# Kernel tuning notes

Hardware: AMD Instinct MI355X
Metric: run time of the kernel (lower is better)

Reference implementation:

```python
import jax, jax.numpy as jnp
import numpy as np

N_NODES = 100000
N_EDGES = 1600000
D = 128
N_LAYERS = 3


def _sage_layer(x, src, dst, Wl, Wr, bias, n_nodes):
    # mean aggregation of source-node features at destination nodes
    msg_sum = jax.ops.segment_sum(x[src], dst, num_segments=n_nodes)  # [N, D]
    cnt = jax.ops.segment_sum(jnp.ones((src.shape[0], 1), x.dtype), dst,
                              num_segments=n_nodes)  # [N, 1]
    mean = msg_sum / jnp.maximum(cnt, 1.0)
    # PyG SAGEConv: out = lin_l(aggr) + lin_r(x); lin_l carries the bias
    return mean @ Wl + x @ Wr + bias


def setup_inputs() -> dict:
    key = jax.random.key(0)
    k1, k2, k3, k4, k5 = jax.random.split(key, 5)
    scale = 1.0 / np.sqrt(D)
    x = jax.random.normal(k1, (N_NODES, D), dtype=jnp.float32)
    edge_index = jax.random.randint(k2, (2, N_EDGES), 0, N_NODES, dtype=jnp.int64)
    W_agg = jax.random.normal(k3, (N_LAYERS, D, D), dtype=jnp.float32) * scale
    W_root = jax.random.normal(k4, (N_LAYERS, D, D), dtype=jnp.float32) * scale
    b = jax.random.normal(k5, (N_LAYERS, D), dtype=jnp.float32) * scale
    return {"x": x, "edge_index": edge_index, "W_agg": W_agg,
            "W_root": W_root, "b": b}


def reference(x, edge_index, W_agg, W_root, b):
    src, dst = edge_index[0], edge_index[1]
    n = x.shape[0]
    # hidden layers: conv -> (dropout=identity in eval) -> relu
    for i in range(N_LAYERS - 1):
        x = _sage_layer(x, src, dst, W_agg[i], W_root[i], b[i], n)
        x = jax.nn.relu(x)
    # final layer: no relu
    x = _sage_layer(x, src, dst, W_agg[-1], W_root[-1], b[-1], n)
    return x
```

## Files before the change

### kernel.cpp

```cpp
#include <hip/hip_runtime.h>
#include <stdint.h>

#define D 128
#define CHUNK 6400

typedef __attribute__((ext_vector_type(8))) __bf16 bf16x8;
typedef __attribute__((ext_vector_type(4))) __bf16 bf16x4;
typedef __attribute__((ext_vector_type(4))) float f32x4;

__global__ void detect_idx(const void* ei, int* flag, int n_nodes) {
    if (blockIdx.x == 0 && threadIdx.x == 0) {
        const long long* p = (const long long*)ei;
        int is64 = 1;
        for (int i = 0; i < 64; ++i) {
            long long v = p[i];
            if (v < 0 || v >= (long long)n_nodes) { is64 = 0; break; }
        }
        *flag = is64;
    }
}

__global__ __launch_bounds__(256) void convert_pack(
        const void* __restrict__ ei, const int* __restrict__ flag,
        unsigned int* __restrict__ eword, unsigned char* __restrict__ gb,
        int* __restrict__ bcnt, int nE) {
    __shared__ int l[256];
    l[threadIdx.x] = 0;
    __syncthreads();
    bool is64 = *flag != 0;
    int stride = gridDim.x * 256;
    for (int e = blockIdx.x * 256 + threadIdx.x; e < nE; e += stride) {
        int s, d;
        if (is64) {
            const long long* p = (const long long*)ei;
            s = (int)p[e];
            d = (int)p[(size_t)nE + e];
        } else {
            const int* p = (const int*)ei;
            s = p[e];
            d = p[nE + e];
        }
        eword[e] = ((unsigned)s << 9) | (unsigned)(d & 511);
        gb[e] = (unsigned char)(d >> 9);
        atomicAdd(&l[d >> 9], 1);
    }
    __syncthreads();
    int v = l[threadIdx.x];
    if (v) atomicAdd(&bcnt[threadIdx.x], v);
}

__global__ void bucket_scan(const int* __restrict__ bcnt, int* __restrict__ bstart,
                            int* __restrict__ bcur, int G, int nE,
                            int* __restrict__ offsets, int n) {
    __shared__ int s[256];
    int t = threadIdx.x;
    int v = (t < G) ? bcnt[t] : 0;
    s[t] = v;
    __syncthreads();
    for (int off = 1; off < 256; off <<= 1) {
        int u = 0;
        if (t >= off) u = s[t - off];
        __syncthreads();
        if (t >= off) s[t] += u;
        __syncthreads();
    }
    if (t < G) { int ex = s[t] - v; bstart[t] = ex; bcur[t] = ex; }
    if (t == 0) offsets[n] = nE;
}

__global__ __launch_bounds__(256) void bucket_fill2(
        const unsigned int* __restrict__ eword, const unsigned char* __restrict__ gb,
        int* __restrict__ bcur, unsigned int* __restrict__ ebuf, int nE) {
    __shared__ unsigned int lw[CHUNK];
    __shared__ unsigned char lg[CHUNK];
    __shared__ int lcnt[256], lbase[256], lcur[256];
    int e0 = blockIdx.x * CHUNK;
    int cnt = nE - e0;
    if (cnt > CHUNK) cnt = CHUNK;
    if (cnt < 0) cnt = 0;
    for (int i = threadIdx.x; i < cnt; i += 256) {
        lw[i] = eword[e0 + i];
        lg[i] = gb[e0 + i];
    }
    lcnt[threadIdx.x] = 0;
    __syncthreads();
    for (int i = threadIdx.x; i < cnt; i += 256)
        atomicAdd(&lcnt[lg[i]], 1);
    __syncthreads();
    int c = lcnt[threadIdx.x];
    if (c > 0) lbase[threadIdx.x] = atomicAdd(&bcur[threadIdx.x], c);
    lcur[threadIdx.x] = 0;
    __syncthreads();
    for (int i = threadIdx.x; i < cnt; i += 256) {
        int g = lg[i];
        int p = lbase[g] + atomicAdd(&lcur[g], 1);
        ebuf[p] = lw[i];
    }
}

__global__ __launch_bounds__(256) void bucket_scatter2(
        const unsigned int* __restrict__ ebuf,
        const int* __restrict__ bstart, const int* __restrict__ bcnt,
        int* __restrict__ offsets, int* __restrict__ csr, int n) {
    __shared__ int ncnt[512], nofs[512], ps[256];
    int g = blockIdx.x;
    int base = bstart[g];
    int cnt = bcnt[g];
    int n0 = g << 9;
    int nr = n - n0; if (nr > 512) nr = 512;
    for (int i = threadIdx.x; i < 512; i += 256) ncnt[i] = 0;
    __syncthreads();
    for (int i = threadIdx.x; i < cnt; i += 256)
        atomicAdd(&ncnt[ebuf[base + i] & 511], 1);
    __syncthreads();
    int t = threadIdx.x;
    int c0 = ncnt[2 * t], c1 = ncnt[2 * t + 1];
    ps[t] = c0 + c1;
    __syncthreads();
    for (int off = 1; off < 256; off <<= 1) {
        int u = 0;
        if (t >= off) u = ps[t - off];
        __syncthreads();
        if (t >= off) ps[t] += u;
        __syncthreads();
    }
    int pex = ps[t] - (c0 + c1);
    nofs[2 * t] = pex;
    nofs[2 * t + 1] = pex + c0;
    __syncthreads();
    for (int i = threadIdx.x; i < nr; i += 256)
        offsets[n0 + i] = base + nofs[i];
    for (int i = threadIdx.x; i < 512; i += 256) ncnt[i] = 0;
    __syncthreads();
    for (int i = threadIdx.x; i < cnt; i += 256) {
        unsigned int w = ebuf[base + i];
        int d = w & 511;
        int p = base + nofs[d] + atomicAdd(&ncnt[d], 1);
        csr[p] = (int)(w >> 9);
    }
}

__global__ void build_wt(const float* __restrict__ Wa, const float* __restrict__ Wr,
                         __bf16* __restrict__ WtHi, __bf16* __restrict__ WtLo) {
    int idx = blockIdx.x * 256 + threadIdx.x;
    if (idx >= 3 * 128 * 256) return;
    int L = idx / (128 * 256);
    int rem = idx % (128 * 256);
    int c = rem / 256;
    int k = rem % 256;
    float v = (k < 128) ? Wa[((size_t)L * 128 + k) * 128 + c]
                        : Wr[((size_t)L * 128 + (k - 128)) * 128 + c];
    __bf16 h = (__bf16)v;
    __bf16 l = (__bf16)(v - (float)h);
    WtHi[idx] = h;
    WtLo[idx] = l;
}

__global__ void cvt_x(const float* __restrict__ x, __bf16* __restrict__ a,
                      int total8) {
    int i = blockIdx.x * 256 + threadIdx.x;
    if (i >= total8) return;
    const float4* p = (const float4*)(x + (size_t)i * 8);
    float4 v0 = p[0], v1 = p[1];
    float vv[8] = {v0.x, v0.y, v0.z, v0.w, v1.x, v1.y, v1.z, v1.w};
    bf16x8 h;
    #pragma unroll
    for (int j = 0; j < 8; ++j) h[j] = (__bf16)vv[j];
    *(bf16x8*)(a + (size_t)i * 8) = h;
}

__global__ __launch_bounds__(256) void quant_act(
        const __bf16* __restrict__ act, unsigned char* __restrict__ q,
        float* __restrict__ scl, int n) {
    int row = (blockIdx.x * blockDim.x + threadIdx.x) >> 4;
    int l8 = (threadIdx.x & 15) << 3;
    if (row >= n) return;
    bf16x8 v = *(const bf16x8*)(act + (size_t)row * D + l8);
    float f[8];
    float m = 0.f;
    #pragma unroll
    for (int j = 0; j < 8; ++j) {
        f[j] = (float)v[j];
        m = fmaxf(m, fabsf(f[j]));
    }
    #pragma unroll
    for (int off = 8; off >= 1; off >>= 1)
        m = fmaxf(m, __shfl_xor(m, off));
    float scale = m * (1.0f / 127.0f);
    float inv = (m > 0.f) ? 127.0f / m : 0.f;
    unsigned int a = 0, b = 0;
    #pragma unroll
    for (int j = 0; j < 4; ++j) {
        unsigned int u = (unsigned int)(__float2int_rn(f[j] * inv) + 128);
        a |= u << (8 * j);
    }
    #pragma unroll
    for (int j = 0; j < 4; ++j) {
        unsigned int u = (unsigned int)(__float2int_rn(f[4 + j] * inv) + 128);
        b |= u << (8 * j);
    }
    *(int2*)(q + (size_t)row * D + l8) = make_int2((int)a, (int)b);
    if ((threadIdx.x & 15) == 0) scl[row] = scale;
}

__global__ __launch_bounds__(256) void agg_mean6(
        const unsigned char* __restrict__ q, const float* __restrict__ scl,
        const int* __restrict__ csr, const int* __restrict__ offs,
        __bf16* __restrict__ mean, int n) {
    int node = (blockIdx.x * blockDim.x + threadIdx.x) >> 4;
    int l8 = (threadIdx.x & 15) << 3;
    if (node >= n) return;
    int beg = offs[node], end = offs[node + 1];
    float acc[8] = {0.f, 0.f, 0.f, 0.f, 0.f, 0.f, 0.f, 0.f};
    float S = 0.f;
    int i = beg;
    for (; i + 8 <= end; i += 8) {
        int2 v[8]; float s[8];
        #pragma unroll
        for (int u = 0; u < 8; ++u) {
            int src = csr[i + u];
            v[u] = *(const int2*)(q + (size_t)src * D + l8);
            s[u] = scl[src];
        }
        #pragma unroll
        for (int u = 0; u < 8; ++u) {
            unsigned int a = (unsigned int)v[u].x, b = (unsigned int)v[u].y;
            float sv = s[u];
            S += sv;
            acc[0] += (float)(a & 255u) * sv;
            acc[1] += (float)((a >> 8) & 255u) * sv;
            acc[2] += (float)((a >> 16) & 255u) * sv;
            acc[3] += (float)(a >> 24) * sv;
            acc[4] += (float)(b & 255u) * sv;
            acc[5] += (float)((b >> 8) & 255u) * sv;
            acc[6] += (float)((b >> 16) & 255u) * sv;
            acc[7] += (float)(b >> 24) * sv;
        }
    }
    for (; i + 4 <= end; i += 4) {
        int2 v[4]; float s[4];
        #pragma unroll
        for (int u = 0; u < 4; ++u) {
            int src = csr[i + u];
            v[u] = *(const int2*)(q + (size_t)src * D + l8);
            s[u] = scl[src];
        }
        #pragma unroll
        for (int u = 0; u < 4; ++u) {
            unsigned int a = (unsigned int)v[u].x, b = (unsigned int)v[u].y;
            float sv = s[u];
            S += sv;
            acc[0] += (float)(a & 255u) * sv;
            acc[1] += (float)((a >> 8) & 255u) * sv;
            acc[2] += (float)((a >> 16) & 255u) * sv;
            acc[3] += (float)(a >> 24) * sv;
            acc[4] += (float)(b & 255u) * sv;
            acc[5] += (float)((b >> 8) & 255u) * sv;
            acc[6] += (float)((b >> 16) & 255u) * sv;
            acc[7] += (float)(b >> 24) * sv;
        }
    }
    for (; i < end; ++i) {
        int src = csr[i];
        int2 v = *(const int2*)(q + (size_t)src * D + l8);
        float sv = scl[src];
        unsigned int a = (unsigned int)v.x, b = (unsigned int)v.y;
        S += sv;
        acc[0] += (float)(a & 255u) * sv;
        acc[1] += (float)((a >> 8) & 255u) * sv;
        acc[2] += (float)((a >> 16) & 255u) * sv;
        acc[3] += (float)(a >> 24) * sv;
        acc[4] += (float)(b & 255u) * sv;
        acc[5] += (float)((b >> 8) & 255u) * sv;
        acc[6] += (float)((b >> 16) & 255u) * sv;
        acc[7] += (float)(b >> 24) * sv;
    }
    int deg = end - beg;
    float inv = 1.0f / (float)(deg > 1 ? deg : 1);
    bf16x8 h;
    #pragma unroll
    for (int j = 0; j < 8; ++j)
        h[j] = (__bf16)((acc[j] - 128.0f * S) * inv);
    *(bf16x8*)(mean + (size_t)node * D + l8) = h;
}

__global__ __launch_bounds__(512, 4) void sage_gemm8(
        const __bf16* __restrict__ mean, const __bf16* __restrict__ act,
        const __bf16* __restrict__ WtHi, const __bf16* __restrict__ WtLo,
        const float* __restrict__ bias,
        __bf16* __restrict__ oB, float* __restrict__ oF,
        int n, int mode, int npairs) {
    __shared__ __align__(16) char sA[2][2][8192];
    __shared__ __align__(16) char sC[2][8192];
    int tid  = threadIdx.x;
    int wave = tid >> 6;
    int lane = tid & 63;
    int r16  = lane & 15;
    int kg   = lane >> 4;
    int colbase = wave * 16;

    bf16x8 BH[8], BL[8];
    #pragma unroll
    for (int c8 = 0; c8 < 8; ++c8) {
        size_t o = (size_t)(colbase + r16) * 256 + c8 * 32 + kg * 8;
        BH[c8] = *(const bf16x8*)(WtHi + o);
        BL[c8] = *(const bf16x8*)(WtLo + o);
    }
    float4 bv = *(const float4*)(bias + colbase + kg * 4);

    int xm = (r16 & 7) << 4;
    int kb[8];
    #pragma unroll
    for (int c8 = 0; c8 < 8; ++c8)
        kb[c8] = r16 * 512 + ((c8 * 64 + kg * 16) ^ xm);

    int srow = tid >> 5;
    int sc16 = tid & 31;
    int sdst = srow * 512 + ((sc16 * 16) ^ ((srow & 7) << 4));

    auto stage_load = [&](int p, int half, int4& r) {
        int grow = p * 32 + half * 16 + srow;
        if (grow < n) {
            const __bf16* src = (sc16 < 16)
                ? (mean + (size_t)grow * D + sc16 * 8)
                : (act  + (size_t)grow * D + (sc16 - 16) * 8);
            r = *(const int4*)src;
        } else {
            r = make_int4(0, 0, 0, 0);
        }
    };

    int pstride = gridDim.x;
    int p = blockIdx.x;

    {
        int4 r0 = make_int4(0,0,0,0), r1 = make_int4(0,0,0,0);
        if (p < npairs) { stage_load(p, 0, r0); stage_load(p, 1, r1); }
        *(int4*)(sA[0][0] + sdst) = r0;
        *(int4*)(sA[0][1] + sdst) = r1;
    }
    __syncthreads();
    int cur = 0;

    for (; p < npairs; p += pstride) {
        int pn = p + pstride;
        bool hasnext = pn < npairs;
        int4 n0, n1;
        if (hasnext) { stage_load(pn, 0, n0); stage_load(pn, 1, n1); }

        f32x4 aH0 = (f32x4){0.f,0.f,0.f,0.f}, aL0 = aH0;
        f32x4 aH1 = aH0, aL1 = aH0;
        const char* b0 = sA[cur][0];
        const char* b1 = sA[cur][1];
        #pragma unroll
        for (int c8 = 0; c8 < 8; ++c8) {
            bf16x8 a0 = *(const bf16x8*)(b0 + kb[c8]);
            bf16x8 a1 = *(const bf16x8*)(b1 + kb[c8]);
            aH0 = __builtin_amdgcn_mfma_f32_16x16x32_bf16(BH[c8], a0, aH0, 0, 0, 0);
            aH1 = __builtin_amdgcn_mfma_f32_16x16x32_bf16(BH[c8], a1, aH1, 0, 0, 0);
            aL0 = __builtin_amdgcn_mfma_f32_16x16x32_bf16(BL[c8], a0, aL0, 0, 0, 0);
            aL1 = __builtin_amdgcn_mfma_f32_16x16x32_bf16(BL[c8], a1, aL1, 0, 0, 0);
        }

        __syncthreads();
        if (hasnext) {
            *(int4*)(sA[cur ^ 1][0] + sdst) = n0;
            *(int4*)(sA[cur ^ 1][1] + sdst) = n1;
        }

        #pragma unroll
        for (int h = 0; h < 2; ++h) {
            f32x4 a = h ? (aH1 + aL1) : (aH0 + aL0);
            float v0 = a[0] + bv.x;
            float v1 = a[1] + bv.y;
            float v2 = a[2] + bv.z;
            float v3 = a[3] + bv.w;
            if (mode == 0) {
                v0 = fmaxf(v0, 0.f); v1 = fmaxf(v1, 0.f);
                v2 = fmaxf(v2, 0.f); v3 = fmaxf(v3, 0.f);
                bf16x4 h4;
                h4[0] = (__bf16)v0; h4[1] = (__bf16)v1;
                h4[2] = (__bf16)v2; h4[3] = (__bf16)v3;
                *(bf16x4*)(sC[h] + r16 * 256 + (colbase + kg * 4) * 2) = h4;
            } else {
                *(f32x4*)(sC[h] + r16 * 512 + (colbase + kg * 4) * 4) =
                    (f32x4){v0, v1, v2, v3};
            }
        }
        __syncthreads();

        if (mode == 0) {
            int rr = tid >> 4, c16 = tid & 15;
            int grow = p * 32 + rr;
            if (grow < n) {
                int4 h = *(const int4*)(sC[rr >> 4] + (rr & 15) * 256 + c16 * 16);
                *(int4*)(oB + (size_t)grow * D + c16 * 8) = h;
            }
        } else {
            #pragma unroll
            for (int pass = 0; pass < 2; ++pass) {
                int chunk = pass * 512 + tid;
                int rr = chunk >> 5, c = chunk & 31;
                int grow = p * 32 + rr;
                if (grow < n) {
                    f32x4 f = *(const f32x4*)(sC[rr >> 4] + (rr & 15) * 512 + c * 16);
                    *(f32x4*)(oF + (size_t)grow * D + c * 4) = f;
                }
            }
        }
        cur ^= 1;
    }
}

extern "C" void kernel_launch(void* const* d_in, const int* in_sizes, int n_in,
                              void* d_out, int out_size, void* d_ws, size_t ws_size,
                              hipStream_t stream) {
    const float* x  = (const float*)d_in[0];
    const void*  ei = d_in[1];
    const float* Wa = (const float*)d_in[2];
    const float* Wr = (const float*)d_in[3];
    const float* bb = (const float*)d_in[4];
    float* outp = (float*)d_out;

    int n  = in_sizes[0] / D;
    int nE = in_sizes[1] / 2;
    int G  = (n + 511) >> 9;

    char* ws = (char*)d_ws;
    size_t off = 0;
    auto alloc = [&](size_t bytes) -> char* {
        char* p = ws + off;
        off = (off + bytes + 255) & ~(size_t)255;
        return p;
    };
    int* flag            = (int*)alloc(4);
    unsigned int* eword  = (unsigned int*)alloc((size_t)nE * 4);
    unsigned char* gbuf  = (unsigned char*)alloc((size_t)nE);
    unsigned int* ebuf   = (unsigned int*)alloc((size_t)nE * 4);
    int* offsets         = (int*)alloc(((size_t)n + 1) * 4);
    int* csr_src         = (int*)alloc((size_t)nE * 4);
    int* bcnt            = (int*)alloc(1024);
    int* bstart          = (int*)alloc(1024);
    int* bcur            = (int*)alloc(1024);
    __bf16* actA         = (__bf16*)alloc((size_t)n * D * 2);
    __bf16* actB         = (__bf16*)alloc((size_t)n * D * 2);
    __bf16* meanP        = (__bf16*)alloc((size_t)n * D * 2);
    unsigned char* qpl   = (unsigned char*)alloc((size_t)n * D);
    float* scl           = (float*)alloc((size_t)n * 4);
    __bf16* WtHi         = (__bf16*)alloc((size_t)3 * 128 * 256 * 2);
    __bf16* WtLo         = (__bf16*)alloc((size_t)3 * 128 * 256 * 2);
    (void)ws_size; (void)n_in; (void)out_size;

    const int B = 256;

    hipLaunchKernelGGL(detect_idx, dim3(1), dim3(64), 0, stream, ei, flag, n);
    hipMemsetAsync(bcnt, 0, 1024, stream);
    hipLaunchKernelGGL(convert_pack, dim3(512), dim3(B), 0, stream,
                       ei, flag, eword, gbuf, bcnt, nE);
    hipLaunchKernelGGL(build_wt, dim3(384), dim3(256), 0, stream, Wa, Wr, WtHi, WtLo);
    int total8 = n * D / 8;
    hipLaunchKernelGGL(cvt_x, dim3((total8 + 255) / 256), dim3(256), 0, stream,
                       x, actA, total8);

    hipLaunchKernelGGL(bucket_scan, dim3(1), dim3(B), 0, stream,
                       bcnt, bstart, bcur, G, nE, offsets, n);
    hipLaunchKernelGGL(bucket_fill2, dim3((nE + CHUNK - 1) / CHUNK), dim3(B), 0, stream,
                       eword, gbuf, bcur, ebuf, nE);
    hipLaunchKernelGGL(bucket_scatter2, dim3(G), dim3(B), 0, stream,
                       ebuf, bstart, bcnt, offsets, csr_src, n);

    int row_blocks = (n * 16 + B - 1) / B;
    int npairs = (n + 31) / 32;
    int gemm_grid = 512;
    const int WSTRIDE = 128 * 256;

    hipLaunchKernelGGL(quant_act, dim3(row_blocks), dim3(B), 0, stream,
                       actA, qpl, scl, n);
    hipLaunchKernelGGL(agg_mean6, dim3(row_blocks), dim3(B), 0, stream,
                       qpl, scl, csr_src, offsets, meanP, n);
    hipLaunchKernelGGL(sage_gemm8, dim3(gemm_grid), dim3(512), 0, stream,
                       meanP, actA, WtHi + 0 * WSTRIDE, WtLo + 0 * WSTRIDE,
                       bb + 0 * D, actB, outp, n, 0, npairs);

    hipLaunchKernelGGL(quant_act, dim3(row_blocks), dim3(B), 0, stream,
                       actB, qpl, scl, n);
    hipLaunchKernelGGL(agg_mean6, dim3(row_blocks), dim3(B), 0, stream,
                       qpl, scl, csr_src, offsets, meanP, n);
    hipLaunchKernelGGL(sage_gemm8, dim3(gemm_grid), dim3(512), 0, stream,
                       meanP, actB, WtHi + 1 * WSTRIDE, WtLo + 1 * WSTRIDE,
                       bb + 1 * D, actA, outp, n, 0, npairs);

    hipLaunchKernelGGL(quant_act, dim3(row_blocks), dim3(B), 0, stream,
                       actA, qpl, scl, n);
    hipLaunchKernelGGL(agg_mean6, dim3(row_blocks), dim3(B), 0, stream,
                       qpl, scl, csr_src, offsets, meanP, n);
    hipLaunchKernelGGL(sage_gemm8, dim3(gemm_grid), dim3(512), 0, stream,
                       meanP, actA, WtHi + 2 * WSTRIDE, WtLo + 2 * WSTRIDE,
                       bb + 2 * D, actB, outp, n, 1, npairs);
}
```

Before: 311.1 us.

## Fuse int8 activation quantization into input conversion and GEMM epilogue

Removes the three standalone quant_act launches. The first quantization now happens inside the fp32-to-bf16 input conversion, and the later ones inside the GEMM's mode-0 epilogue, which quantizes the bf16 tile it has just written. This avoids re-reading each layer's activations from global memory and the extra launch overhead. It also XOR-swizzles the epilogue's shared-memory staging buffer to cut LDS bank conflicts, at the cost of extra ALU work in the GEMM epilogue.

```diff
diff --git a/kernel.cpp b/kernel.cpp
--- a/kernel.cpp
+++ b/kernel.cpp
@@ -156,51 +156,39 @@
     WtLo[idx] = l;
 }
 
-__global__ void cvt_x(const float* __restrict__ x, __bf16* __restrict__ a,
-                      int total8) {
+__global__ __launch_bounds__(256) void cvt_x_q(
+        const float* __restrict__ x, __bf16* __restrict__ a,
+        unsigned char* __restrict__ q, float* __restrict__ scl, int total8) {
     int i = blockIdx.x * 256 + threadIdx.x;
     if (i >= total8) return;
+    int row = i >> 4;
+    int c16 = i & 15;
     const float4* p = (const float4*)(x + (size_t)i * 8);
     float4 v0 = p[0], v1 = p[1];
     float vv[8] = {v0.x, v0.y, v0.z, v0.w, v1.x, v1.y, v1.z, v1.w};
     bf16x8 h;
-    #pragma unroll
-    for (int j = 0; j < 8; ++j) h[j] = (__bf16)vv[j];
+    float f[8], m = 0.f;
+    #pragma unroll
+    for (int j = 0; j < 8; ++j) {
+        h[j] = (__bf16)vv[j];
+        f[j] = (float)h[j];
+        m = fmaxf(m, fabsf(f[j]));
+    }
     *(bf16x8*)(a + (size_t)i * 8) = h;
-}
-
-__global__ __launch_bounds__(256) void quant_act(
-        const __bf16* __restrict__ act, unsigned char* __restrict__ q,
-        float* __restrict__ scl, int n) {
-    int row = (blockIdx.x * blockDim.x + threadIdx.x) >> 4;
-    int l8 = (threadIdx.x & 15) << 3;
-    if (row >= n) return;
-    bf16x8 v = *(const bf16x8*)(act + (size_t)row * D + l8);
-    float f[8];
-    float m = 0.f;
-    #pragma unroll
-    for (int j = 0; j < 8; ++j) {
-        f[j] = (float)v[j];
-        m = fmaxf(m, fabsf(f[j]));
-    }
     #pragma unroll
     for (int off = 8; off >= 1; off >>= 1)
         m = fmaxf(m, __shfl_xor(m, off));
     float scale = m * (1.0f / 127.0f);
     float inv = (m > 0.f) ? 127.0f / m : 0.f;
-    unsigned int a = 0, b = 0;
-    #pragma unroll
-    for (int j = 0; j < 4; ++j) {
-        unsigned int u = (unsigned int)(__float2int_rn(f[j] * inv) + 128);
-        a |= u << (8 * j);
-    }
-    #pragma unroll
-    for (int j = 0; j < 4; ++j) {
-        unsigned int u = (unsigned int)(__float2int_rn(f[4 + j] * inv) + 128);
-        b |= u << (8 * j);
-    }
-    *(int2*)(q + (size_t)row * D + l8) = make_int2((int)a, (int)b);
-    if ((threadIdx.x & 15) == 0) scl[row] = scale;
+    unsigned int pa = 0, pb = 0;
+    #pragma unroll
+    for (int j = 0; j < 4; ++j)
+        pa |= (unsigned int)(__float2int_rn(f[j] * inv) + 128) << (8 * j);
+    #pragma unroll
+    for (int j = 0; j < 4; ++j)
+        pb |= (unsigned int)(__float2int_rn(f[4 + j] * inv) + 128) << (8 * j);
+    *(int2*)(q + (size_t)row * D + c16 * 8) = make_int2((int)pa, (int)pb);
+    if (c16 == 0) scl[row] = scale;
 }
 
 __global__ __launch_bounds__(256) void agg_mean6(
@@ -284,11 +272,12 @@
     *(bf16x8*)(mean + (size_t)node * D + l8) = h;
 }
 
-__global__ __launch_bounds__(512, 4) void sage_gemm8(
+__global__ __launch_bounds__(512, 4) void sage_gemm8b(
         const __bf16* __restrict__ mean, const __bf16* __restrict__ act,
         const __bf16* __restrict__ WtHi, const __bf16* __restrict__ WtLo,
         const float* __restrict__ bias,
         __bf16* __restrict__ oB, float* __restrict__ oF,
+        unsigned char* __restrict__ qpl, float* __restrict__ scl,
         int n, int mode, int npairs) {
     __shared__ __align__(16) char sA[2][2][8192];
     __shared__ __align__(16) char sC[2][8192];
@@ -381,9 +370,11 @@
                 bf16x4 h4;
                 h4[0] = (__bf16)v0; h4[1] = (__bf16)v1;
                 h4[2] = (__bf16)v2; h4[3] = (__bf16)v3;
-                *(bf16x4*)(sC[h] + r16 * 256 + (colbase + kg * 4) * 2) = h4;
+                *(bf16x4*)(sC[h] + r16 * 256 +
+                           (((colbase + kg * 4) * 2) ^ xm)) = h4;
             } else {
-                *(f32x4*)(sC[h] + r16 * 512 + (colbase + kg * 4) * 4) =
+                *(f32x4*)(sC[h] + r16 * 512 +
+                          (((colbase + kg * 4) * 4) ^ xm)) =
                     (f32x4){v0, v1, v2, v3};
             }
         }
@@ -392,9 +383,34 @@
         if (mode == 0) {
             int rr = tid >> 4, c16 = tid & 15;
             int grow = p * 32 + rr;
+            int row = rr & 15;
             if (grow < n) {
-                int4 h = *(const int4*)(sC[rr >> 4] + (rr & 15) * 256 + c16 * 16);
-                *(int4*)(oB + (size_t)grow * D + c16 * 8) = h;
+                int4 hc = *(const int4*)(sC[rr >> 4] + row * 256 +
+                                         ((c16 * 16) ^ ((row & 7) << 4)));
+                *(int4*)(oB + (size_t)grow * D + c16 * 8) = hc;
+                const unsigned short* hs = (const unsigned short*)&hc;
+                float f[8], m = 0.f;
+                #pragma unroll
+                for (int j = 0; j < 8; ++j) {
+                    unsigned int bits = (unsigned int)hs[j] << 16;
+                    f[j] = __uint_as_float(bits);
+                    m = fmaxf(m, fabsf(f[j]));
+                }
+                #pragma unroll
+                for (int off = 8; off >= 1; off >>= 1)
+                    m = fmaxf(m, __shfl_xor(m, off));
+                float scale = m * (1.0f / 127.0f);
+                float inv = (m > 0.f) ? 127.0f / m : 0.f;
+                unsigned int pa = 0, pb = 0;
+                #pragma unroll
+                for (int j = 0; j < 4; ++j)
+                    pa |= (unsigned int)(__float2int_rn(f[j] * inv) + 128) << (8 * j);
+                #pragma unroll
+                for (int j = 0; j < 4; ++j)
+                    pb |= (unsigned int)(__float2int_rn(f[4 + j] * inv) + 128) << (8 * j);
+                *(int2*)(qpl + (size_t)grow * D + c16 * 8) =
+                    make_int2((int)pa, (int)pb);
+                if (c16 == 0) scl[grow] = scale;
             }
         } else {
             #pragma unroll
@@ -402,8 +418,10 @@
                 int chunk = pass * 512 + tid;
                 int rr = chunk >> 5, c = chunk & 31;
                 int grow = p * 32 + rr;
+                int row = rr & 15;
                 if (grow < n) {
-                    f32x4 f = *(const f32x4*)(sC[rr >> 4] + (rr & 15) * 512 + c * 16);
+                    f32x4 f = *(const f32x4*)(sC[rr >> 4] + row * 512 +
+                                              ((c * 16) ^ ((row & 7) << 4)));
                     *(f32x4*)(oF + (size_t)grow * D + c * 4) = f;
                 }
             }
@@ -459,8 +477,8 @@
                        ei, flag, eword, gbuf, bcnt, nE);
     hipLaunchKernelGGL(build_wt, dim3(384), dim3(256), 0, stream, Wa, Wr, WtHi, WtLo);
     int total8 = n * D / 8;
-    hipLaunchKernelGGL(cvt_x, dim3((total8 + 255) / 256), dim3(256), 0, stream,
-                       x, actA, total8);
+    hipLaunchKernelGGL(cvt_x_q, dim3((total8 + 255) / 256), dim3(256), 0, stream,
+                       x, actA, qpl, scl, total8);
 
     hipLaunchKernelGGL(bucket_scan, dim3(1), dim3(B), 0, stream,
                        bcnt, bstart, bcur, G, nE, offsets, n);
@@ -474,27 +492,21 @@
     int gemm_grid = 512;
     const int WSTRIDE = 128 * 256;
 
-    hipLaunchKernelGGL(quant_act, dim3(row_blocks), dim3(B), 0, stream,
-                       actA, qpl, scl, n);
     hipLaunchKernelGGL(agg_mean6, dim3(row_blocks), dim3(B), 0, stream,
                        qpl, scl, csr_src, offsets, meanP, n);
-    hipLaunchKernelGGL(sage_gemm8, dim3(gemm_grid), dim3(512), 0, stream,
+    hipLaunchKernelGGL(sage_gemm8b, dim3(gemm_grid), dim3(512), 0, stream,
                        meanP, actA, WtHi + 0 * WSTRIDE, WtLo + 0 * WSTRIDE,
-                       bb + 0 * D, actB, outp, n, 0, npairs);
-
-    hipLaunchKernelGGL(quant_act, dim3(row_blocks), dim3(B), 0, stream,
-                       actB, qpl, scl, n);
+                       bb + 0 * D, actB, outp, qpl, scl, n, 0, npairs);
+
     hipLaunchKernelGGL(agg_mean6, dim3(row_blocks), dim3(B), 0, stream,
                        qpl, scl, csr_src, offsets, meanP, n);
-    hipLaunchKernelGGL(sage_gemm8, dim3(gemm_grid), dim3(512), 0, stream,
+    hipLaunchKernelGGL(sage_gemm8b, dim3(gemm_grid), dim3(512), 0, stream,
                        meanP, actB, WtHi + 1 * WSTRIDE, WtLo + 1 * WSTRIDE,
-                       bb + 1 * D, actA, outp, n, 0, npairs);
-
-    hipLaunchKernelGGL(quant_act, dim3(row_blocks), dim3(B), 0, stream,
-                       actA, qpl, scl, n);
+                       bb + 1 * D, actA, outp, qpl, scl, n, 0, npairs);
+
     hipLaunchKernelGGL(agg_mean6, dim3(row_blocks), dim3(B), 0, stream,
                        qpl, scl, csr_src, offsets, meanP, n);
-    hipLaunchKernelGGL(sage_gemm8, dim3(gemm_grid), dim3(512), 0, stream,
+    hipLaunchKernelGGL(sage_gemm8b, dim3(gemm_grid), dim3(512), 0, stream,
                        meanP, actA, WtHi + 2 * WSTRIDE, WtLo + 2 * WSTRIDE,
-                       bb + 2 * D, actB, outp, n, 1, npairs);
-}
+                       bb + 2 * D, actB, outp, qpl, scl, n, 1, npairs);
+}
```

Result: faster. 296.4 us (median of 2 runs) (-4.7%).
